# Optimization experiments

Measured on AMD Instinct MI355X. Metric: run time of the kernel, lower is better.

## Reference

```python
import jax, jax.numpy as jnp
import numpy as np

NODE_DIM, EDGE_DIM, HIDDEN = 1, 2, 64
N_NODES, N_EDGES = 50000, 1000000
MASK_FILL = -1e9


def setup_inputs() -> dict:
    key = jax.random.key(0)
    ks = jax.random.split(key, 10)
    x = jax.random.normal(ks[0], (N_NODES, NODE_DIM), dtype=jnp.float32)
    edge_index = jax.random.randint(ks[1], (2, N_EDGES), 0, N_NODES, dtype=jnp.int64)
    edge_attr = jax.random.normal(ks[2], (N_EDGES, EDGE_DIM), dtype=jnp.float32)
    edge_mask = jax.random.randint(ks[3], (N_EDGES,), 0, 2) > 0
    fin = 2 * NODE_DIM + EDGE_DIM  # 4
    s1 = 1.0 / np.sqrt(fin)
    s2 = 1.0 / np.sqrt(HIDDEN)
    W1 = jax.random.uniform(ks[4], (fin, HIDDEN), jnp.float32, -s1, s1)
    b1 = jax.random.uniform(ks[5], (HIDDEN,), jnp.float32, -s1, s1)
    W2 = jax.random.uniform(ks[6], (HIDDEN, HIDDEN), jnp.float32, -s2, s2)
    b2 = jax.random.uniform(ks[7], (HIDDEN,), jnp.float32, -s2, s2)
    Ws = jax.random.uniform(ks[8], (HIDDEN, 1), jnp.float32, -s2, s2)
    bs = jax.random.uniform(ks[9], (1,), jnp.float32, -s2, s2)
    return {"x": x, "edge_index": edge_index, "edge_attr": edge_attr,
            "edge_mask": edge_mask, "W1": W1, "b1": b1, "W2": W2, "b2": b2,
            "Ws": Ws, "bs": bs}


def reference(x, edge_index, edge_attr, edge_mask, W1, b1, W2, b2, Ws, bs):
    row, col = edge_index[0], edge_index[1]
    # gather src/dst node features and concat with edge_attr -> [E, 4]
    edge_input = jnp.concatenate([x[row], x[col], edge_attr], axis=1)
    h = jax.nn.relu(edge_input @ W1 + b1)   # [E, H]
    edge_emb = h @ W2 + b2                   # [E, H]
    scores = (edge_emb @ Ws + bs)[:, 0]      # [E]
    scores = jnp.where(edge_mask, scores, jnp.float32(MASK_FILL))
    return scores
```

## Files before the change

kernel.cpp:

```cpp
#include <hip/hip_runtime.h>

#define HIDDEN 64
#define MASK_FILL -1e9f
#define EPT 4

__global__ __launch_bounds__(256) void edge_score_fused(
    const float* __restrict__ x,
    const int* __restrict__ edge_index,
    const float* __restrict__ edge_attr,
    const int* __restrict__ edge_mask,
    const float* __restrict__ W1,
    const float* __restrict__ b1,
    const float* __restrict__ W2,
    const float* __restrict__ b2,
    const float* __restrict__ Ws,
    const float* __restrict__ bs,
    float* __restrict__ out, int E)
{
    __shared__ float4 wPack[HIDDEN];
    __shared__ float2 bv[HIDDEN];
    __shared__ float  cS;

    const int t = threadIdx.x;

    {
        const float4* W2v = reinterpret_cast<const float4*>(W2 + t * 16);
        const int j0 = 16 * (t & 3);
        float p = 0.f;
#pragma unroll
        for (int i = 0; i < 4; ++i) {
            const float4 wv = W2v[i];
            const int j = j0 + 4 * i;
            p = fmaf(wv.x, Ws[j],     p);
            p = fmaf(wv.y, Ws[j + 1], p);
            p = fmaf(wv.z, Ws[j + 2], p);
            p = fmaf(wv.w, Ws[j + 3], p);
        }
        p += __shfl_xor(p, 1);
        p += __shfl_xor(p, 2);
        if ((t & 3) == 0) bv[t >> 2].y = p;
    }
    if (t < 64) {
        wPack[t] = make_float4(W1[t], W1[64 + t], W1[128 + t], W1[192 + t]);
        bv[t].x = b1[t];
    } else if (t < 128) {
        const int l = t - 64;
        float p = b2[l] * Ws[l];
#pragma unroll
        for (int off = 1; off < 64; off <<= 1) p += __shfl_xor(p, off);
        if (l == 0) cS = p + bs[0];
    }
    __syncthreads();

    const int tid = blockIdx.x * 256 + t;
    const int e = tid * EPT;
    if (e >= E) return;

    const int4 rows = *reinterpret_cast<const int4*>(edge_index + e);
    const int4 cols = *reinterpret_cast<const int4*>(edge_index + E + e);
    const int4 mk   = *reinterpret_cast<const int4*>(edge_mask + e);
    const float4 eaA = *reinterpret_cast<const float4*>(edge_attr + 2 * e);
    const float4 eaB = *reinterpret_cast<const float4*>(edge_attr + 2 * e + 4);

    const float xr0 = x[rows.x], xr1 = x[rows.y], xr2 = x[rows.z], xr3 = x[rows.w];
    const float xc0 = x[cols.x], xc1 = x[cols.y], xc2 = x[cols.z], xc3 = x[cols.w];

    const float c = cS;
    float s0 = c, s1 = c, s2 = c, s3 = c;

#pragma unroll 4
    for (int k = 0; k < HIDDEN; ++k) {
        const float4 w  = wPack[k];
        const float2 bk = bv[k];

        float h0 = fmaf(xr0, w.x, fmaf(xc0, w.y, fmaf(eaA.x, w.z, fmaf(eaA.y, w.w, bk.x))));
        float h1 = fmaf(xr1, w.x, fmaf(xc1, w.y, fmaf(eaA.z, w.z, fmaf(eaA.w, w.w, bk.x))));
        float h2 = fmaf(xr2, w.x, fmaf(xc2, w.y, fmaf(eaB.x, w.z, fmaf(eaB.y, w.w, bk.x))));
        float h3 = fmaf(xr3, w.x, fmaf(xc3, w.y, fmaf(eaB.z, w.z, fmaf(eaB.w, w.w, bk.x))));
        s0 = fmaf(fmaxf(h0, 0.f), bk.y, s0);
        s1 = fmaf(fmaxf(h1, 0.f), bk.y, s1);
        s2 = fmaf(fmaxf(h2, 0.f), bk.y, s2);
        s3 = fmaf(fmaxf(h3, 0.f), bk.y, s3);
    }

    float4 res;
    res.x = mk.x ? s0 : MASK_FILL;
    res.y = mk.y ? s1 : MASK_FILL;
    res.z = mk.z ? s2 : MASK_FILL;
    res.w = mk.w ? s3 : MASK_FILL;
    *reinterpret_cast<float4*>(out + e) = res;
}

extern "C" void kernel_launch(void* const* d_in, const int* in_sizes, int n_in,
                              void* d_out, int out_size, void* d_ws, size_t ws_size,
                              hipStream_t stream) {
    const float* x          = (const float*)d_in[0];
    const int*   edge_index = (const int*)d_in[1];
    const float* edge_attr  = (const float*)d_in[2];
    const int*   edge_mask  = (const int*)d_in[3];
    const float* W1 = (const float*)d_in[4];
    const float* b1 = (const float*)d_in[5];
    const float* W2 = (const float*)d_in[6];
    const float* b2 = (const float*)d_in[7];
    const float* Ws = (const float*)d_in[8];
    const float* bs = (const float*)d_in[9];
    float* out = (float*)d_out;

    const int E = out_size;
    const int threads = 256;
    const int work = (E + EPT - 1) / EPT;
    const int blocks = (work + threads - 1) / threads;
    edge_score_fused<<<blocks, threads, 0, stream>>>(
        x, edge_index, edge_attr, edge_mask, W1, b1, W2, b2, Ws, bs, out, E);
}
```

Measured before the change: 21.31 us.

## Pack hidden units in pairs for packed-FMA math and use nontemporal edge loads

```diff
diff --git a/kernel.cpp b/kernel.cpp
--- a/kernel.cpp
+++ b/kernel.cpp
@@ -1,4 +1,8 @@
 #include <hip/hip_runtime.h>
+
+typedef float f2 __attribute__((ext_vector_type(2)));
+typedef float f4 __attribute__((ext_vector_type(4)));
+typedef int   i4 __attribute__((ext_vector_type(4)));
 
 #define HIDDEN 64
 #define MASK_FILL -1e9f
@@ -17,38 +21,43 @@
     const float* __restrict__ bs,
     float* __restrict__ out, int E)
 {
-    __shared__ float4 wPack[HIDDEN];
-    __shared__ float2 bv[HIDDEN];
-    __shared__ float  cS;
+    __shared__ f4 wA[32], wB[32], wC[32];
+    __shared__ float cS;
 
     const int t = threadIdx.x;
 
     {
-        const float4* W2v = reinterpret_cast<const float4*>(W2 + t * 16);
+        const f4* W2v = reinterpret_cast<const f4*>(W2 + t * 16);
         const int j0 = 16 * (t & 3);
         float p = 0.f;
 #pragma unroll
         for (int i = 0; i < 4; ++i) {
-            const float4 wv = W2v[i];
+            const f4 wv = W2v[i];
             const int j = j0 + 4 * i;
-            p = fmaf(wv.x, Ws[j],     p);
+            p = fmaf(wv.x, Ws[j], p);
             p = fmaf(wv.y, Ws[j + 1], p);
             p = fmaf(wv.z, Ws[j + 2], p);
             p = fmaf(wv.w, Ws[j + 3], p);
         }
         p += __shfl_xor(p, 1);
         p += __shfl_xor(p, 2);
-        if ((t & 3) == 0) bv[t >> 2].y = p;
+        if ((t & 3) == 0) {
+            const int k = t >> 2;
+            reinterpret_cast<float*>(&wC[k >> 1])[2 + (k & 1)] = p;
+        }
     }
-    if (t < 64) {
-        wPack[t] = make_float4(W1[t], W1[64 + t], W1[128 + t], W1[192 + t]);
-        bv[t].x = b1[t];
-    } else if (t < 128) {
+    if (t < 32) {
+        wA[t] = (f4){W1[2 * t], W1[2 * t + 1], W1[64 + 2 * t], W1[64 + 2 * t + 1]};
+        wB[t] = (f4){W1[128 + 2 * t], W1[128 + 2 * t + 1], W1[192 + 2 * t], W1[192 + 2 * t + 1]};
+    } else if (t >= 64 && t < 128) {
         const int l = t - 64;
         float p = b2[l] * Ws[l];
 #pragma unroll
         for (int off = 1; off < 64; off <<= 1) p += __shfl_xor(p, off);
         if (l == 0) cS = p + bs[0];
+    } else if (t >= 192) {
+        const int k = t - 192;
+        reinterpret_cast<float*>(&wC[k >> 1])[k & 1] = b1[k];
     }
     __syncthreads();
 
@@ -56,39 +65,54 @@
     const int e = tid * EPT;
     if (e >= E) return;
 
-    const int4 rows = *reinterpret_cast<const int4*>(edge_index + e);
-    const int4 cols = *reinterpret_cast<const int4*>(edge_index + E + e);
-    const int4 mk   = *reinterpret_cast<const int4*>(edge_mask + e);
-    const float4 eaA = *reinterpret_cast<const float4*>(edge_attr + 2 * e);
-    const float4 eaB = *reinterpret_cast<const float4*>(edge_attr + 2 * e + 4);
+    const i4 rows = __builtin_nontemporal_load(reinterpret_cast<const i4*>(edge_index + e));
+    const i4 cols = __builtin_nontemporal_load(reinterpret_cast<const i4*>(edge_index + E + e));
+    const i4 mk   = __builtin_nontemporal_load(reinterpret_cast<const i4*>(edge_mask + e));
+    const f4 eaA  = __builtin_nontemporal_load(reinterpret_cast<const f4*>(edge_attr + 2 * e));
+    const f4 eaB  = __builtin_nontemporal_load(reinterpret_cast<const f4*>(edge_attr + 2 * e + 4));
 
-    const float xr0 = x[rows.x], xr1 = x[rows.y], xr2 = x[rows.z], xr3 = x[rows.w];
-    const float xc0 = x[cols.x], xc1 = x[cols.y], xc2 = x[cols.z], xc3 = x[cols.w];
+    const f2 xr0 = {x[rows.x], x[rows.x]}, xr1 = {x[rows.y], x[rows.y]},
+             xr2 = {x[rows.z], x[rows.z]}, xr3 = {x[rows.w], x[rows.w]};
+    const f2 xc0 = {x[cols.x], x[cols.x]}, xc1 = {x[cols.y], x[cols.y]},
+             xc2 = {x[cols.z], x[cols.z]}, xc3 = {x[cols.w], x[cols.w]};
+    const f2 e00 = {eaA.x, eaA.x}, e10 = {eaA.y, eaA.y};
+    const f2 e01 = {eaA.z, eaA.z}, e11 = {eaA.w, eaA.w};
+    const f2 e02 = {eaB.x, eaB.x}, e12 = {eaB.y, eaB.y};
+    const f2 e03 = {eaB.z, eaB.z}, e13 = {eaB.w, eaB.w};
 
     const float c = cS;
-    float s0 = c, s1 = c, s2 = c, s3 = c;
+    const f2 z2 = {0.f, 0.f};
+    f2 a0 = {c, 0.f}, a1 = {c, 0.f}, a2 = {c, 0.f}, a3 = {c, 0.f};
 
 #pragma unroll 4
-    for (int k = 0; k < HIDDEN; ++k) {
-        const float4 w  = wPack[k];
-        const float2 bk = bv[k];
+    for (int k2 = 0; k2 < 32; ++k2) {
+        const f4 A = wA[k2];
+        const f4 B = wB[k2];
+        const f4 C = wC[k2];
+        const f2 w0 = {A.x, A.y}, w1 = {A.z, A.w};
+        const f2 w2 = {B.x, B.y}, w3 = {B.z, B.w};
+        const f2 bb = {C.x, C.y}, vv = {C.z, C.w};
 
-        float h0 = fmaf(xr0, w.x, fmaf(xc0, w.y, fmaf(eaA.x, w.z, fmaf(eaA.y, w.w, bk.x))));
-        float h1 = fmaf(xr1, w.x, fmaf(xc1, w.y, fmaf(eaA.z, w.z, fmaf(eaA.w, w.w, bk.x))));
-        float h2 = fmaf(xr2, w.x, fmaf(xc2, w.y, fmaf(eaB.x, w.z, fmaf(eaB.y, w.w, bk.x))));
-        float h3 = fmaf(xr3, w.x, fmaf(xc3, w.y, fmaf(eaB.z, w.z, fmaf(eaB.w, w.w, bk.x))));
-        s0 = fmaf(fmaxf(h0, 0.f), bk.y, s0);
-        s1 = fmaf(fmaxf(h1, 0.f), bk.y, s1);
-        s2 = fmaf(fmaxf(h2, 0.f), bk.y, s2);
-        s3 = fmaf(fmaxf(h3, 0.f), bk.y, s3);
+        f2 h0 = __builtin_elementwise_fma(xr0, w0, __builtin_elementwise_fma(xc0, w1,
+                __builtin_elementwise_fma(e00, w2, __builtin_elementwise_fma(e10, w3, bb))));
+        f2 h1 = __builtin_elementwise_fma(xr1, w0, __builtin_elementwise_fma(xc1, w1,
+                __builtin_elementwise_fma(e01, w2, __builtin_elementwise_fma(e11, w3, bb))));
+        f2 h2 = __builtin_elementwise_fma(xr2, w0, __builtin_elementwise_fma(xc2, w1,
+                __builtin_elementwise_fma(e02, w2, __builtin_elementwise_fma(e12, w3, bb))));
+        f2 h3 = __builtin_elementwise_fma(xr3, w0, __builtin_elementwise_fma(xc3, w1,
+                __builtin_elementwise_fma(e03, w2, __builtin_elementwise_fma(e13, w3, bb))));
+        a0 = __builtin_elementwise_fma(__builtin_elementwise_max(h0, z2), vv, a0);
+        a1 = __builtin_elementwise_fma(__builtin_elementwise_max(h1, z2), vv, a1);
+        a2 = __builtin_elementwise_fma(__builtin_elementwise_max(h2, z2), vv, a2);
+        a3 = __builtin_elementwise_fma(__builtin_elementwise_max(h3, z2), vv, a3);
     }
 
-    float4 res;
-    res.x = mk.x ? s0 : MASK_FILL;
-    res.y = mk.y ? s1 : MASK_FILL;
-    res.z = mk.z ? s2 : MASK_FILL;
-    res.w = mk.w ? s3 : MASK_FILL;
-    *reinterpret_cast<float4*>(out + e) = res;
+    f4 res;
+    res.x = mk.x ? (a0.x + a0.y) : MASK_FILL;
+    res.y = mk.y ? (a1.x + a1.y) : MASK_FILL;
+    res.z = mk.z ? (a2.x + a2.y) : MASK_FILL;
+    res.w = mk.w ? (a3.x + a3.y) : MASK_FILL;
+    __builtin_nontemporal_store(res, reinterpret_cast<f4*>(out + e));
 }
 
 extern "C" void kernel_launch(void* const* d_in, const int* in_sizes, int n_in,
```

Measured after the change: 19.60 us. 8.0% less time.
